# Kernel optimization log

Measured on AMD Instinct MI355X. Metric: run time of the kernel, lower is better.

## Reference

```python
import jax, jax.numpy as jnp
import numpy as np

N = 100000          # nodes
E = 6400000         # edges (avg degree 64)
V0 = 1.0            # self.v0 (source assigns v0 despite u0 arg)
W0 = 1.0            # self.w0
EPS = 1e-12         # torch F.normalize eps


def setup_inputs() -> dict:
    key = jax.random.key(0)
    k1, k2, k3, k4 = jax.random.split(key, 4)
    return {
        "x": jax.random.normal(k1, (N, 1), dtype=jnp.float32),
        "theta": jax.random.normal(k2, (N, 1), dtype=jnp.float32),
        "edge_src": jax.random.randint(k3, (E,), 0, N, dtype=jnp.int64),
        "edge_dst": jax.random.randint(k4, (E,), 0, N, dtype=jnp.int64),
    }


def reference(x, theta, edge_src, edge_dst):
    # node velocity: v = v0 * [cos(theta), sin(theta)]  -> [N, 2]
    v = V0 * jnp.concatenate([jnp.cos(theta), jnp.sin(theta)], axis=-1)

    # per-edge message: dtheta = x[src] - theta[dst]; m = [cos, sin]  -> [E, 2]
    dtheta = x[edge_src] - theta[edge_dst]            # [E, 1]
    msg = jnp.concatenate([jnp.cos(dtheta), jnp.sin(dtheta)], axis=-1)  # [E, 2]

    # mailbox mean over incoming edges per dst node (segment mean)
    seg_sum = jax.ops.segment_sum(msg, edge_dst, num_segments=N)               # [N, 2]
    cnt = jax.ops.segment_sum(jnp.ones((E, 1), msg.dtype), edge_dst, num_segments=N)
    mean_cs = seg_sum / jnp.maximum(cnt, 1.0)

    # torque: w = w0 * normalize(mean_cs)[..., 1:2]  (L2-normalize, torch eps)
    norm = jnp.maximum(jnp.linalg.norm(mean_cs, axis=-1, keepdims=True), EPS)
    w = W0 * (mean_cs / norm)[..., 1:2]               # [N, 1]

    # updated ndata packed as [v_x, v_y, w]
    return jnp.concatenate([v, w], axis=-1)           # [N, 3]
```

## Files before the change

### kernel.cpp

```cpp
#include <hip/hip_runtime.h>
#include <math.h>


#define EPS 1e-12f
#define NPART 16
#define RNODES 6250
#define RMAX 6250
#define BLK 1024

#define NBIN 1024
#define BINBLK 512
#define CAP 512
#define TILE 2048
#define BUF 256
#define OCAP 262144

static __device__ __forceinline__ unsigned long long pack_cs(float xv) {
    float sn, cs;
    __sincosf(xv, &sn, &cs);
    const int ci = __float2int_rn(cs * 32768.0f);
    const int si = __float2int_rn(sn * 32768.0f);
    return (1ull << 52)
         | ((unsigned long long)(unsigned)(si + 32768) << 26)
         | (unsigned long long)(unsigned)(ci + 32768);
}

__global__ __launch_bounds__(256) void prep_pack_kernel(
        const float* __restrict__ x,
        unsigned long long* __restrict__ pu, int N) {
    int i = blockIdx.x * blockDim.x + threadIdx.x;
    if (i < N) pu[i] = pack_cs(x[i]);
}

__global__ __launch_bounds__(BINBLK, 8) void bin_kernel(
        const float* __restrict__ x,
        const int* __restrict__ esrc,
        const int* __restrict__ edst,
        unsigned long long* __restrict__ pu,
        unsigned* __restrict__ records,
        int* __restrict__ counts,
        unsigned long long* __restrict__ oflow,
        int* __restrict__ oflow_cnt,
        int E, int N) {
    __shared__ unsigned stage[NPART * BUF];
    __shared__ int scur[NPART];
    __shared__ int gcur[NPART];

    {
        const int PPB = (N + NBIN) / NBIN;
        const int idx = blockIdx.x * PPB + threadIdx.x;
        if (threadIdx.x < PPB && idx <= N)
            pu[idx] = (idx < N) ? pack_cs(x[idx]) : 0ull;
    }
    if (threadIdx.x < NPART) { scur[threadIdx.x] = 0; gcur[threadIdx.x] = 0; }
    __syncthreads();

    const int chunk = (((E + NBIN - 1) / NBIN) + 3) & ~3;
    const int beg = blockIdx.x * chunk;
    const int end = min(beg + chunk, E);
    unsigned* __restrict__ myrec =
        records + (size_t)blockIdx.x * (NPART * CAP);
    const int wave = threadIdx.x >> 6;
    const int lane = threadIdx.x & 63;

#define BIN_ONE(dd, ss) do {                                              \
        const unsigned d_ = (unsigned)(dd);                               \
        const unsigned p_ = d_ / RNODES;         \
        const unsigned dl_ = d_ - p_ * RNODES;         \
        const unsigned rec_ = ((unsigned)(ss) << 13) | dl_;               \
        const int slot_ = atomicAdd(&scur[p_], 1);                        \
        if (slot_ < BUF) {                                                \
            stage[p_ * BUF + slot_] = rec_;                               \
        } else {                                                          \
            const int pos_ = gcur[p_] + slot_;      \
            if (pos_ < CAP) myrec[p_ * CAP + pos_] = rec_;                \
            else {                                                        \
                const int g_ = atomicAdd(oflow_cnt, 1);                   \
                if (g_ < OCAP)                                            \
                    oflow[g_] = ((unsigned long long)(unsigned)(ss) << 32)\
                              | d_;                                       \
            }                                                             \
        }                                                                 \
    } while (0)

    for (int tbeg = beg; tbeg < end; tbeg += TILE) {
        const int i = tbeg + threadIdx.x * 4;
        if (i + 4 <= end) {
            const int4 d4 = *(const int4*)&edst[i];
            const int4 s4 = *(const int4*)&esrc[i];
            BIN_ONE(d4.x, s4.x);
            BIN_ONE(d4.y, s4.y);
            BIN_ONE(d4.z, s4.z);
            BIN_ONE(d4.w, s4.w);
        } else {
            for (int k = i; k < end; ++k) BIN_ONE(edst[k], esrc[k]);
        }
        __syncthreads();
        #pragma unroll
        for (int q = 0; q < 2; ++q) {
            const int p = wave * 2 + q;
            const int sc = scur[p];
            const int gc = gcur[p];
            const int cpy = min(min(sc, (int)BUF), max((int)CAP - gc, 0));
            for (int k = lane; k < cpy; k += 64)
                myrec[p * CAP + gc + k] = stage[p * BUF + k];
            if (lane == 0) {
                gcur[p] = min(gc + sc, (int)CAP);
                scur[p] = 0;
            }
        }
        __syncthreads();
    }
#undef BIN_ONE

    if (threadIdx.x < NPART) {
        const int c = min(gcur[threadIdx.x], (int)CAP);
        const int c8 = min((c + 7) & ~7, (int)CAP);
        for (int k = c; k < c8; ++k)
            myrec[threadIdx.x * CAP + k] = ((unsigned)N << 13);
        counts[blockIdx.x * NPART + threadIdx.x] = c8;
    }
}

__global__ __launch_bounds__(BLK, 2) void accum_kernel(
        const unsigned long long* __restrict__ pu,
        const unsigned* __restrict__ records,
        const int* __restrict__ counts,
        const unsigned long long* __restrict__ oflow,
        const int* __restrict__ oflow_cnt,
        unsigned long long* __restrict__ partials,
        int nslice) {
    __shared__ unsigned long long lacc[RMAX];
    const int p = blockIdx.x / nslice;
    const int s = blockIdx.x % nslice;

    for (int k = threadIdx.x; k < RNODES; k += BLK) lacc[k] = 0ull;
    __syncthreads();

    const int wave = threadIdx.x >> 6;
    const int lane = threadIdx.x & 63;
    const int wstep = (BLK / 64) * nslice;
    for (int c = s + wave * nslice; c < NBIN; c += wstep) {
        const int cnt = counts[c * NPART + p];
        const unsigned* __restrict__ base =
            records + ((size_t)(c * NPART + p)) * CAP;
        for (int i = lane * 8; i < cnt; i += 64 * 8) {
            const uint4 ra = *(const uint4*)&base[i];
            const uint4 rb = *(const uint4*)&base[i + 4];
            const unsigned long long v0 = pu[ra.x >> 13];
            const unsigned long long v1 = pu[ra.y >> 13];
            const unsigned long long v2 = pu[ra.z >> 13];
            const unsigned long long v3 = pu[ra.w >> 13];
            const unsigned long long v4 = pu[rb.x >> 13];
            const unsigned long long v5 = pu[rb.y >> 13];
            const unsigned long long v6 = pu[rb.z >> 13];
            const unsigned long long v7 = pu[rb.w >> 13];
            atomicAdd(&lacc[ra.x & 8191], v0);
            atomicAdd(&lacc[ra.y & 8191], v1);
            atomicAdd(&lacc[ra.z & 8191], v2);
            atomicAdd(&lacc[ra.w & 8191], v3);
            atomicAdd(&lacc[rb.x & 8191], v4);
            atomicAdd(&lacc[rb.y & 8191], v5);
            atomicAdd(&lacc[rb.z & 8191], v6);
            atomicAdd(&lacc[rb.w & 8191], v7);
        }
    }

    if (s == 0) {
        const int oc = min(*oflow_cnt, (int)OCAP);
        const unsigned pBeg = (unsigned)(p * RNODES);
        for (int i = threadIdx.x; i < oc; i += BLK) {
            const unsigned long long e = oflow[i];
            const unsigned dl = (unsigned)e - pBeg;
            if (dl < (unsigned)RNODES) atomicAdd(&lacc[dl], pu[e >> 32]);
        }
    }

    __syncthreads();
    unsigned long long* dst = partials + (size_t)blockIdx.x * RNODES;
    for (int k = threadIdx.x; k < RNODES; k += BLK) dst[k] = lacc[k];
}

__global__ __launch_bounds__(BLK, 2) void scatter_kernel(
        const unsigned long long* __restrict__ pu,
        const int* __restrict__ esrc,
        const int* __restrict__ edst,
        unsigned long long* __restrict__ partials,
        int E, int R, int nslice) {
    __shared__ unsigned long long lacc[RMAX];
    const int p = blockIdx.x / nslice;
    const int s = blockIdx.x % nslice;
    const int pBeg = p * R;

    for (int k = threadIdx.x; k < R; k += BLK) lacc[k] = 0ull;
    __syncthreads();

    const int per = (((E + nslice - 1) / nslice) + 7) & ~7;
    const int beg = s * per;
    const int end = min(beg + per, E);
    const int end8 = beg + (max(end - beg, 0) & ~7);

    for (int i = beg + threadIdx.x * 8; i < end8; i += BLK * 8) {
        const int4 da = *(const int4*)&edst[i];
        const int4 db = *(const int4*)&edst[i + 4];
        const int4 sa = *(const int4*)&esrc[i];
        const int4 sb = *(const int4*)&esrc[i + 4];
        const unsigned dl0 = (unsigned)(da.x - pBeg);
        const unsigned dl1 = (unsigned)(da.y - pBeg);
        const unsigned dl2 = (unsigned)(da.z - pBeg);
        const unsigned dl3 = (unsigned)(da.w - pBeg);
        const unsigned dl4 = (unsigned)(db.x - pBeg);
        const unsigned dl5 = (unsigned)(db.y - pBeg);
        const unsigned dl6 = (unsigned)(db.z - pBeg);
        const unsigned dl7 = (unsigned)(db.w - pBeg);
        const bool h0 = dl0 < (unsigned)R, h1 = dl1 < (unsigned)R;
        const bool h2 = dl2 < (unsigned)R, h3 = dl3 < (unsigned)R;
        const bool h4 = dl4 < (unsigned)R, h5 = dl5 < (unsigned)R;
        const bool h6 = dl6 < (unsigned)R, h7 = dl7 < (unsigned)R;
        unsigned long long v0 = 0, v1 = 0, v2 = 0, v3 = 0;
        unsigned long long v4 = 0, v5 = 0, v6 = 0, v7 = 0;
        if (h0) v0 = pu[sa.x];
        if (h1) v1 = pu[sa.y];
        if (h2) v2 = pu[sa.z];
        if (h3) v3 = pu[sa.w];
        if (h4) v4 = pu[sb.x];
        if (h5) v5 = pu[sb.y];
        if (h6) v6 = pu[sb.z];
        if (h7) v7 = pu[sb.w];
        if (h0) atomicAdd(&lacc[dl0], v0);
        if (h1) atomicAdd(&lacc[dl1], v1);
        if (h2) atomicAdd(&lacc[dl2], v2);
        if (h3) atomicAdd(&lacc[dl3], v3);
        if (h4) atomicAdd(&lacc[dl4], v4);
        if (h5) atomicAdd(&lacc[dl5], v5);
        if (h6) atomicAdd(&lacc[dl6], v6);
        if (h7) atomicAdd(&lacc[dl7], v7);
    }
    for (int i = end8 + threadIdx.x; i < end; i += BLK) {
        const unsigned dl = (unsigned)(edst[i] - pBeg);
        if (dl < (unsigned)R) atomicAdd(&lacc[dl], pu[esrc[i]]);
    }

    __syncthreads();
    unsigned long long* dst = partials + (size_t)blockIdx.x * R;
    for (int k = threadIdx.x; k < R; k += BLK) dst[k] = lacc[k];
}

__global__ __launch_bounds__(256) void reduce_kernel(
        const float* __restrict__ theta,
        const unsigned long long* __restrict__ partials,
        float* __restrict__ out, int N, int R, int nslice) {
    const int n = blockIdx.x * blockDim.x + threadIdx.x;
    if (n >= N) return;
    const int p = n / R;
    const int j = n - p * R;
    const unsigned long long* base = partials + (size_t)p * nslice * R + j;
    unsigned long long t = 0ull;
    #pragma unroll 8
    for (int s = 0; s < nslice; ++s) t += base[(size_t)s * R];
    const long long k  = (long long)(t >> 52);
    const long long cf = (long long)(t & 0x3FFFFFFull);
    const long long sf = (long long)((t >> 26) & 0x3FFFFFFull);
    const float C  = (float)(cf - k * 32768) * (1.0f / 32768.0f);
    const float Sv = (float)(sf - k * 32768) * (1.0f / 32768.0f);
    float sn, cs;
    __sincosf(theta[n], &sn, &cs);
    const float nrm = fmaxf(sqrtf(C * C + Sv * Sv), EPS);
    out[3 * n + 0] = cs;
    out[3 * n + 1] = sn;
    out[3 * n + 2] = (cs * Sv - sn * C) / nrm;
}

__global__ __launch_bounds__(256) void prep_acc_kernel(float2* __restrict__ acc, int N) {
    int i = blockIdx.x * blockDim.x + threadIdx.x;
    if (i < N) acc[i] = make_float2(0.0f, 0.0f);
}

__global__ __launch_bounds__(256) void edge_scatter_sincos_kernel(
        const int* __restrict__ esrc,
        const int* __restrict__ edst,
        const float* __restrict__ x,
        float2* __restrict__ acc, int E) {
    const int i = (blockIdx.x * 256 + threadIdx.x) * 4;
    float* accf = (float*)acc;
    for (int k = i; k < min(i + 4, E); ++k) {
        float sn, cs;
        __sincosf(x[esrc[k]], &sn, &cs);
        const int d = edst[k];
        unsafeAtomicAdd(&accf[2 * d],     cs);
        unsafeAtomicAdd(&accf[2 * d + 1], sn);
    }
}

__global__ __launch_bounds__(256) void node_kernel(
        const float* __restrict__ theta,
        const float2* __restrict__ acc,
        float* __restrict__ out, int N) {
    int n = blockIdx.x * blockDim.x + threadIdx.x;
    if (n >= N) return;
    float sn, cs;
    __sincosf(theta[n], &sn, &cs);
    const float2 a = acc[n];
    const float nrm = fmaxf(sqrtf(a.x * a.x + a.y * a.y), EPS);
    out[3 * n + 0] = cs;
    out[3 * n + 1] = sn;
    out[3 * n + 2] = (cs * a.y - sn * a.x) / nrm;
}

extern "C" void kernel_launch(void* const* d_in, const int* in_sizes, int n_in,
                              void* d_out, int out_size, void* d_ws, size_t ws_size,
                              hipStream_t stream) {
    const float* x     = (const float*)d_in[0];
    const float* theta = (const float*)d_in[1];
    const int*   esrc  = (const int*)d_in[2];
    const int*   edst  = (const int*)d_in[3];
    float*       out   = (float*)d_out;

    const int N = in_sizes[0];
    const int E = in_sizes[2];

    if (N <= NPART * RNODES && (size_t)(N + 1) <= (size_t)NBIN * BINBLK) {
        const int nslice = 32;
        const size_t part_bytes = (size_t)NPART * nslice * RNODES * 8ull;
        const size_t pu_bytes   = (((size_t)(N + 1) * 8ull) + 15) & ~(size_t)15;
        const size_t rec_bytes  = (size_t)NBIN * NPART * CAP * 4ull;
        const size_t cnt_bytes  = (size_t)NBIN * NPART * 4ull;
        const size_t ofc_bytes  = 64;
        const size_t ofl_bytes  = (size_t)OCAP * 8ull;
        const size_t total = part_bytes + pu_bytes + rec_bytes + cnt_bytes
                           + ofc_bytes + ofl_bytes;
        if (ws_size >= total) {
            char* w = (char*)d_ws;
            unsigned long long* partials = (unsigned long long*)w; w += part_bytes;
            unsigned long long* pu       = (unsigned long long*)w; w += pu_bytes;
            unsigned*           records  = (unsigned*)w;           w += rec_bytes;
            int*                counts   = (int*)w;                w += cnt_bytes;
            int*                oflow_cnt= (int*)w;                w += ofc_bytes;
            unsigned long long* oflow    = (unsigned long long*)w;

            hipMemsetAsync(oflow_cnt, 0, sizeof(int), stream);
            bin_kernel<<<NBIN, BINBLK, 0, stream>>>(
                x, esrc, edst, pu, records, counts, oflow, oflow_cnt, E, N);
            accum_kernel<<<NPART * nslice, BLK, 0, stream>>>(
                pu, records, counts, oflow, oflow_cnt, partials, nslice);
            reduce_kernel<<<(N + 255) / 256, 256, 0, stream>>>(
                theta, partials, out, N, RNODES, nslice);
            return;
        }
    }

    {
        const int R = (N + NPART - 1) / NPART;
        const size_t pu_bytes = (size_t)N * sizeof(unsigned long long);
        if (R <= RMAX) {
            for (int nslice : {32, 16, 8}) {
                const size_t part_bytes =
                    (size_t)NPART * nslice * R * sizeof(unsigned long long);
                if (ws_size >= part_bytes + pu_bytes) {
                    unsigned long long* partials = (unsigned long long*)d_ws;
                    unsigned long long* pu =
                        (unsigned long long*)((char*)d_ws + part_bytes);
                    prep_pack_kernel<<<(N + 255) / 256, 256, 0, stream>>>(
                        x, pu, N);
                    scatter_kernel<<<NPART * nslice, BLK, 0, stream>>>(
                        pu, esrc, edst, partials, E, R, nslice);
                    reduce_kernel<<<(N + 255) / 256, 256, 0, stream>>>(
                        theta, partials, out, N, R, nslice);
                    return;
                }
            }
        }
    }

    float2* acc = (float2*)d_ws;
    prep_acc_kernel<<<(N + 255) / 256, 256, 0, stream>>>(acc, N);
    edge_scatter_sincos_kernel<<<(E + 1023) / 1024, 256, 0, stream>>>(esrc, edst, x, acc, E);
    node_kernel<<<(N + 255) / 256, 256, 0, stream>>>(theta, acc, out, N);
}
```

Measured before the change: 139.2 us.

## Replace per-block fixed-capacity record bins with sharded global regions via atomic reservation

The binning kernel no longer writes each block's records into fixed per-block, per-partition slots with counts. It now reserves space with a global atomic in one of 8 shards per partition and appends the staged records contiguously there, padded to multiples of 8. The accumulation kernel then streams each shard's contiguous region split evenly across slices, instead of walking 1024 small per-block bins of uneven length. The tile is also doubled to 8 edges per thread. This should improve load balance and memory coalescing, at the cost of global atomic reservations and larger shared staging buffers.

```diff
diff --git a/kernel.cpp b/kernel.cpp
--- a/kernel.cpp
+++ b/kernel.cpp
@@ -10,9 +10,10 @@
 
 #define NBIN 1024
 #define BINBLK 512
-#define CAP 512
-#define TILE 2048
-#define BUF 256
+#define TILE 4096
+#define BUF 512
+#define NSHARD 8
+#define SCAP 57344
 #define OCAP 262144
 
 static __device__ __forceinline__ unsigned long long pack_cs(float xv) {
@@ -37,14 +38,12 @@
         const int* __restrict__ esrc,
         const int* __restrict__ edst,
         unsigned long long* __restrict__ pu,
-        unsigned* __restrict__ records,
-        int* __restrict__ counts,
+        unsigned* __restrict__ rreg,
+        int* __restrict__ gctrl,
         unsigned long long* __restrict__ oflow,
-        int* __restrict__ oflow_cnt,
         int E, int N) {
     __shared__ unsigned stage[NPART * BUF];
     __shared__ int scur[NPART];
-    __shared__ int gcur[NPART];
 
     {
         const int PPB = (N + NBIN) / NBIN;
@@ -52,14 +51,14 @@
         if (threadIdx.x < PPB && idx <= N)
             pu[idx] = (idx < N) ? pack_cs(x[idx]) : 0ull;
     }
-    if (threadIdx.x < NPART) { scur[threadIdx.x] = 0; gcur[threadIdx.x] = 0; }
-    __syncthreads();
-
-    const int chunk = (((E + NBIN - 1) / NBIN) + 3) & ~3;
+    if (threadIdx.x < NPART) scur[threadIdx.x] = 0;
+    __syncthreads();
+
+    const int chunk = (((E + NBIN - 1) / NBIN) + 7) & ~7;
     const int beg = blockIdx.x * chunk;
     const int end = min(beg + chunk, E);
-    unsigned* __restrict__ myrec =
-        records + (size_t)blockIdx.x * (NPART * CAP);
+    const int shard = blockIdx.x & (NSHARD - 1);
+    int* __restrict__ oflow_cnt = gctrl + 128;
     const int wave = threadIdx.x >> 6;
     const int lane = threadIdx.x & 63;
 
@@ -71,63 +70,70 @@
         const int slot_ = atomicAdd(&scur[p_], 1);                        \
         if (slot_ < BUF) {                                                \
             stage[p_ * BUF + slot_] = rec_;                               \
-        } else {                                                          \
-            const int pos_ = gcur[p_] + slot_;      \
-            if (pos_ < CAP) myrec[p_ * CAP + pos_] = rec_;                \
-            else {                                                        \
-                const int g_ = atomicAdd(oflow_cnt, 1);                   \
-                if (g_ < OCAP)                                            \
-                    oflow[g_] = ((unsigned long long)(unsigned)(ss) << 32)\
-                              | d_;                                       \
-            }                                                             \
+        } else {                                      \
+            const int g_ = atomicAdd(oflow_cnt, 1);                       \
+            if (g_ < OCAP)                                                \
+                oflow[g_] = ((unsigned long long)(unsigned)(ss) << 32)    \
+                          | d_;                                           \
         }                                                                 \
     } while (0)
 
     for (int tbeg = beg; tbeg < end; tbeg += TILE) {
-        const int i = tbeg + threadIdx.x * 4;
-        if (i + 4 <= end) {
-            const int4 d4 = *(const int4*)&edst[i];
-            const int4 s4 = *(const int4*)&esrc[i];
-            BIN_ONE(d4.x, s4.x);
-            BIN_ONE(d4.y, s4.y);
-            BIN_ONE(d4.z, s4.z);
-            BIN_ONE(d4.w, s4.w);
+        const int i = tbeg + threadIdx.x * 8;
+        if (i + 8 <= end) {
+            const int4 da = *(const int4*)&edst[i];
+            const int4 db = *(const int4*)&edst[i + 4];
+            const int4 sa = *(const int4*)&esrc[i];
+            const int4 sb = *(const int4*)&esrc[i + 4];
+            BIN_ONE(da.x, sa.x);
+            BIN_ONE(da.y, sa.y);
+            BIN_ONE(da.z, sa.z);
+            BIN_ONE(da.w, sa.w);
+            BIN_ONE(db.x, sb.x);
+            BIN_ONE(db.y, sb.y);
+            BIN_ONE(db.z, sb.z);
+            BIN_ONE(db.w, sb.w);
         } else {
-            for (int k = i; k < end; ++k) BIN_ONE(edst[k], esrc[k]);
+            for (int k = i; k < min(i + 8, end); ++k)
+                BIN_ONE(edst[k], esrc[k]);
         }
         __syncthreads();
         #pragma unroll
         for (int q = 0; q < 2; ++q) {
             const int p = wave * 2 + q;
-            const int sc = scur[p];
-            const int gc = gcur[p];
-            const int cpy = min(min(sc, (int)BUF), max((int)CAP - gc, 0));
-            for (int k = lane; k < cpy; k += 64)
-                myrec[p * CAP + gc + k] = stage[p * BUF + k];
-            if (lane == 0) {
-                gcur[p] = min(gc + sc, (int)CAP);
-                scur[p] = 0;
+            const int sc = min(scur[p], (int)BUF);
+            if (sc > 0) {
+                const int rsv = (sc + 7) & ~7;
+                int rb = 0;
+                if (lane == 0)
+                    rb = atomicAdd(&gctrl[p * NSHARD + shard], rsv);
+                rb = __shfl(rb, 0);
+                unsigned* __restrict__ dst =
+                    rreg + (size_t)(p * NSHARD + shard) * SCAP;
+                const int fit = min(rsv, max((int)SCAP - rb, 0));
+                for (int k = lane; k < fit; k += 64)
+                    dst[rb + k] = (k < sc) ? stage[p * BUF + k]
+                                           : ((unsigned)N << 13);
+                for (int k = fit + lane; k < sc; k += 64) {
+                    const unsigned rec = stage[p * BUF + k];
+                    const int g = atomicAdd(oflow_cnt, 1);
+                    if (g < OCAP)
+                        oflow[g] = ((unsigned long long)(rec >> 13) << 32)
+                                 | (unsigned)(p * RNODES + (rec & 8191u));
+                }
             }
+            if (lane == 0) scur[p] = 0;
         }
         __syncthreads();
     }
 #undef BIN_ONE
-
-    if (threadIdx.x < NPART) {
-        const int c = min(gcur[threadIdx.x], (int)CAP);
-        const int c8 = min((c + 7) & ~7, (int)CAP);
-        for (int k = c; k < c8; ++k)
-            myrec[threadIdx.x * CAP + k] = ((unsigned)N << 13);
-        counts[blockIdx.x * NPART + threadIdx.x] = c8;
-    }
 }
 
 __global__ __launch_bounds__(BLK, 2) void accum_kernel(
         const unsigned long long* __restrict__ pu,
-        const unsigned* __restrict__ records,
-        const int* __restrict__ counts,
+        const unsigned* __restrict__ rreg,
+        const int* __restrict__ gctrl,
         const unsigned long long* __restrict__ oflow,
-        const int* __restrict__ oflow_cnt,
         unsigned long long* __restrict__ partials,
         int nslice) {
     __shared__ unsigned long long lacc[RMAX];
@@ -139,35 +145,38 @@
 
     const int wave = threadIdx.x >> 6;
     const int lane = threadIdx.x & 63;
-    const int wstep = (BLK / 64) * nslice;
-    for (int c = s + wave * nslice; c < NBIN; c += wstep) {
-        const int cnt = counts[c * NPART + p];
-        const unsigned* __restrict__ base =
-            records + ((size_t)(c * NPART + p)) * CAP;
-        for (int i = lane * 8; i < cnt; i += 64 * 8) {
-            const uint4 ra = *(const uint4*)&base[i];
-            const uint4 rb = *(const uint4*)&base[i + 4];
-            const unsigned long long v0 = pu[ra.x >> 13];
-            const unsigned long long v1 = pu[ra.y >> 13];
-            const unsigned long long v2 = pu[ra.z >> 13];
-            const unsigned long long v3 = pu[ra.w >> 13];
-            const unsigned long long v4 = pu[rb.x >> 13];
-            const unsigned long long v5 = pu[rb.y >> 13];
-            const unsigned long long v6 = pu[rb.z >> 13];
-            const unsigned long long v7 = pu[rb.w >> 13];
-            atomicAdd(&lacc[ra.x & 8191], v0);
-            atomicAdd(&lacc[ra.y & 8191], v1);
-            atomicAdd(&lacc[ra.z & 8191], v2);
-            atomicAdd(&lacc[ra.w & 8191], v3);
-            atomicAdd(&lacc[rb.x & 8191], v4);
-            atomicAdd(&lacc[rb.y & 8191], v5);
-            atomicAdd(&lacc[rb.z & 8191], v6);
-            atomicAdd(&lacc[rb.w & 8191], v7);
-        }
+    const int shard = wave >> 1;
+    const int sub = wave & 1;
+
+    const int cnt = min(gctrl[p * NSHARD + shard], (int)SCAP);
+    const unsigned* __restrict__ base =
+        rreg + (size_t)(p * NSHARD + shard) * SCAP;
+    const int per = (((cnt + nslice - 1) / nslice) + 7) & ~7;
+    const int sbeg = s * per;
+    const int send = min(sbeg + per, cnt);
+    for (int i = sbeg + (sub * 64 + lane) * 8; i < send; i += 128 * 8) {
+        const uint4 ra = *(const uint4*)&base[i];
+        const uint4 rb4 = *(const uint4*)&base[i + 4];
+        const unsigned long long v0 = pu[ra.x >> 13];
+        const unsigned long long v1 = pu[ra.y >> 13];
+        const unsigned long long v2 = pu[ra.z >> 13];
+        const unsigned long long v3 = pu[ra.w >> 13];
+        const unsigned long long v4 = pu[rb4.x >> 13];
+        const unsigned long long v5 = pu[rb4.y >> 13];
+        const unsigned long long v6 = pu[rb4.z >> 13];
+        const unsigned long long v7 = pu[rb4.w >> 13];
+        atomicAdd(&lacc[ra.x & 8191], v0);
+        atomicAdd(&lacc[ra.y & 8191], v1);
+        atomicAdd(&lacc[ra.z & 8191], v2);
+        atomicAdd(&lacc[ra.w & 8191], v3);
+        atomicAdd(&lacc[rb4.x & 8191], v4);
+        atomicAdd(&lacc[rb4.y & 8191], v5);
+        atomicAdd(&lacc[rb4.z & 8191], v6);
+        atomicAdd(&lacc[rb4.w & 8191], v7);
     }
 
     if (s == 0) {
-        const int oc = min(*oflow_cnt, (int)OCAP);
+        const int oc = min(gctrl[128], (int)OCAP);
         const unsigned pBeg = (unsigned)(p * RNODES);
         for (int i = threadIdx.x; i < oc; i += BLK) {
             const unsigned long long e = oflow[i];
@@ -319,30 +328,29 @@
     const int N = in_sizes[0];
     const int E = in_sizes[2];
 
-    if (N <= NPART * RNODES && (size_t)(N + 1) <= (size_t)NBIN * BINBLK) {
+    if (N <= NPART * RNODES && N < (1 << 19)
+        && (size_t)(N + 1) <= (size_t)NBIN * BINBLK) {
         const int nslice = 32;
         const size_t part_bytes = (size_t)NPART * nslice * RNODES * 8ull;
         const size_t pu_bytes   = (((size_t)(N + 1) * 8ull) + 15) & ~(size_t)15;
-        const size_t rec_bytes  = (size_t)NBIN * NPART * CAP * 4ull;
-        const size_t cnt_bytes  = (size_t)NBIN * NPART * 4ull;
-        const size_t ofc_bytes  = 64;
+        const size_t rreg_bytes = (size_t)NPART * NSHARD * SCAP * 4ull;
+        const size_t ctl_bytes  = 1024;
         const size_t ofl_bytes  = (size_t)OCAP * 8ull;
-        const size_t total = part_bytes + pu_bytes + rec_bytes + cnt_bytes
-                           + ofc_bytes + ofl_bytes;
+        const size_t total = part_bytes + pu_bytes + rreg_bytes + ctl_bytes
+                           + ofl_bytes;
         if (ws_size >= total) {
             char* w = (char*)d_ws;
             unsigned long long* partials = (unsigned long long*)w; w += part_bytes;
             unsigned long long* pu       = (unsigned long long*)w; w += pu_bytes;
-            unsigned*           records  = (unsigned*)w;           w += rec_bytes;
-            int*                counts   = (int*)w;                w += cnt_bytes;
-            int*                oflow_cnt= (int*)w;                w += ofc_bytes;
+            unsigned*           rreg     = (unsigned*)w;           w += rreg_bytes;
+            int*                gctrl    = (int*)w;                w += ctl_bytes;
             unsigned long long* oflow    = (unsigned long long*)w;
 
-            hipMemsetAsync(oflow_cnt, 0, sizeof(int), stream);
+            hipMemsetAsync(gctrl, 0, ctl_bytes, stream);
             bin_kernel<<<NBIN, BINBLK, 0, stream>>>(
-                x, esrc, edst, pu, records, counts, oflow, oflow_cnt, E, N);
+                x, esrc, edst, pu, rreg, gctrl, oflow, E, N);
             accum_kernel<<<NPART * nslice, BLK, 0, stream>>>(
-                pu, records, counts, oflow, oflow_cnt, partials, nslice);
+                pu, rreg, gctrl, oflow, partials, nslice);
             reduce_kernel<<<(N + 255) / 256, 256, 0, stream>>>(
                 theta, partials, out, N, RNODES, nslice);
             return;
```

Result: slower. 204.9 us (+47.2%).
